# Performance work log

Hardware: AMD Instinct MI355X
Metric: run time of the kernel (lower is better)

The kernel has to match this reference:

```python
import jax, jax.numpy as jnp
import numpy as np

B, N, H = 8, 2048, 1024
FF = 4 * H
EPS = 1e-5

def layer_norm(x, g, b):
    mu = jnp.mean(x, axis=-1, keepdims=True)
    var = jnp.mean(jnp.square(x - mu), axis=-1, keepdims=True)
    return (x - mu) * jax.lax.rsqrt(var + EPS) * g + b

def setup_inputs() -> dict:
    key = jax.random.key(0)
    ks = jax.random.split(key, 6)
    s1 = 1.0 / np.sqrt(H)
    s2 = 1.0 / np.sqrt(FF)
    return {
        "x": jax.random.normal(ks[0], (B, N, H), dtype=jnp.float32),
        "ln1_g": jnp.ones((H,), jnp.float32),
        "ln1_b": jnp.zeros((H,), jnp.float32),
        "ln2_g": jnp.ones((H,), jnp.float32),
        "ln2_b": jnp.zeros((H,), jnp.float32),
        "w1": jax.random.uniform(ks[1], (H, FF), jnp.float32, -s1, s1),
        "b1": jax.random.uniform(ks[2], (FF,), jnp.float32, -s1, s1),
        "w2": jax.random.uniform(ks[3], (FF, H), jnp.float32, -s2, s2),
        "b2": jax.random.uniform(ks[4], (H,), jnp.float32, -s2, s2),
    }

def reference(x, ln1_g, ln1_b, ln2_g, ln2_b, w1, b1, w2, b2):
    # raw unscaled self-attention: softmax(x x^T) x  (dropout = identity, eval mode)
    scores = jnp.einsum('bnh,bmh->bnm', x, x)          # [B,N,N]
    attn = jax.nn.softmax(scores, axis=-1)
    attended = jnp.einsum('bnm,bmh->bnh', attn, x)     # [B,N,H]
    h = layer_norm(x + attended, ln1_g, ln1_b)
    ffn = jnp.einsum('bnf,fh->bnh', jax.nn.gelu(jnp.einsum('bnh,hf->bnf', h, w1) + b1, approximate=False), w2) + b2
    return layer_norm(h + ffn, ln2_g, ln2_b)
```

## Files before the change

### kernel.cpp

```cpp
#include <hip/hip_runtime.h>
#include <stdint.h>

#define NB 8
#define NN 2048
#define HH 1024
#define FFD 4096
constexpr float EPS_ = 1e-5f;

typedef _Float16 f16;
typedef _Float16 f16x8 __attribute__((ext_vector_type(8)));
typedef float f32x4 __attribute__((ext_vector_type(4)));

__device__ __forceinline__ f32x4 MFMA(f16x8 a, f16x8 b, f32x4 c) {
  return __builtin_amdgcn_mfma_f32_16x16x32_f16(a, b, c, 0, 0, 0);
}
__device__ __forceinline__ ushort h2u(f16 h) { union { f16 h; ushort u; } v; v.h = h; return v.u; }
__device__ __forceinline__ uint pack2(float a, float b) {
  return (uint)h2u((f16)a) | ((uint)h2u((f16)b) << 16);
}
__device__ __forceinline__ float4 ld4(const float* p) { return *(const float4*)p; }
__device__ __forceinline__ float gelu(float u) {
  return 0.5f * u * (1.0f + erff(u * 0.70710678118654752f));
}

__global__ void transpose_f16(const float* __restrict__ src, f16* __restrict__ dst,
                              int R, int C) {
  __shared__ float tl[32][33];
  const int t = threadIdx.x;
  const int c0 = blockIdx.x * 32, r0 = blockIdx.y * 32;
  {
    const int r = t >> 3, c4 = t & 7;
    float4 v = ld4(src + (size_t)(r0 + r) * C + c0 + c4 * 4);
    tl[r][c4 * 4 + 0] = v.x; tl[r][c4 * 4 + 1] = v.y;
    tl[r][c4 * 4 + 2] = v.z; tl[r][c4 * 4 + 3] = v.w;
  }
  __syncthreads();
  {
    const int c = t >> 3, r4 = t & 7;
    ushort4 o;
    o.x = h2u((f16)tl[r4 * 4 + 0][c]);
    o.y = h2u((f16)tl[r4 * 4 + 1][c]);
    o.z = h2u((f16)tl[r4 * 4 + 2][c]);
    o.w = h2u((f16)tl[r4 * 4 + 3][c]);
    *(ushort4*)(dst + (size_t)(c0 + c) * R + r0 + r4 * 4) = o;
  }
}

__global__ __launch_bounds__(1024)
void attn_kernel(const float* __restrict__ x, const float* __restrict__ g1,
                 const float* __restrict__ lb1, float* __restrict__ hout) {
  extern __shared__ char smem[];
  char* AB = smem;
  char* BB = smem + 5120;
  char* PB = smem + 46080;
  char* VB = smem + 62976;
  float* RD  = (float*)(smem + 144896);
  float* RD2 = (float*)(smem + 145920);

  const int t = threadIdx.x, l = t & 63, w = t >> 6;
  const int lg = l >> 4, li = l & 15;
  const int wr = w >> 3, wc = w & 7;
  const int b = blockIdx.y, m0 = blockIdx.x * 32;
  const float* __restrict__ xb = x + (size_t)b * NN * HH;

  const int ar = t >> 5, ak = t & 31;
  const int bj = t >> 2, bq = t & 3;
  const int vjp = t & 15, vhg = t >> 4;

  f32x4 Oacc[8] = {};
  float m_run[4] = {-INFINITY, -INFINITY, -INFINITY, -INFINITY};
  float l_run[4] = {0.f, 0.f, 0.f, 0.f};

  for (int jt = 0; jt < 8; ++jt) {
    const int j0 = jt * 256;
    f32x4 sacc[2] = {};
    float qv = xb[(size_t)(m0 + ar) * HH + ak];
    float4 ca = ld4(xb + (size_t)(j0 + bj) * HH + bq * 8);
    float4 cb = ld4(xb + (size_t)(j0 + bj) * HH + bq * 8 + 4);
    for (int kc = 0; kc < 32; ++kc) {
      __syncthreads();
      {
        f16 qh = (f16)qv; f16 ql = (f16)(qv - (float)qh);
        *(ushort*)(AB + ar * 80 + ak * 2) = h2u(qh);
        *(ushort*)(AB + 2560 + ar * 80 + ak * 2) = h2u(ql);
        float vv[8] = {ca.x, ca.y, ca.z, ca.w, cb.x, cb.y, cb.z, cb.w};
        f16x8 hi8, lo8;
#pragma unroll
        for (int i = 0; i < 8; ++i) {
          f16 h = (f16)vv[i]; hi8[i] = h; lo8[i] = (f16)(vv[i] - (float)h);
        }
        *(f16x8*)(BB + bj * 80 + bq * 16) = hi8;
        *(f16x8*)(BB + 20480 + bj * 80 + bq * 16) = lo8;
      }
      if (kc < 31) {
        const int k0 = (kc + 1) * 32;
        qv = xb[(size_t)(m0 + ar) * HH + k0 + ak];
        ca = ld4(xb + (size_t)(j0 + bj) * HH + k0 + bq * 8);
        cb = ld4(xb + (size_t)(j0 + bj) * HH + k0 + bq * 8 + 4);
      }
      __syncthreads();
      const int arow = wr * 16 + li;
      f16x8 ahi = *(const f16x8*)(AB + arow * 80 + lg * 16);
      f16x8 alo = *(const f16x8*)(AB + 2560 + arow * 80 + lg * 16);
#pragma unroll
      for (int ct = 0; ct < 2; ++ct) {
        const int j = wc * 32 + ct * 16 + li;
        f16x8 bhi = *(const f16x8*)(BB + j * 80 + lg * 16);
        f16x8 blo = *(const f16x8*)(BB + 20480 + j * 80 + lg * 16);
        sacc[ct] = MFMA(ahi, bhi, sacc[ct]);
        sacc[ct] = MFMA(ahi, blo, sacc[ct]);
        sacc[ct] = MFMA(alo, bhi, sacc[ct]);
      }
    }

    float tm[4];
#pragma unroll
    for (int r = 0; r < 4; ++r) tm[r] = fmaxf(sacc[0][r], sacc[1][r]);
#pragma unroll
    for (int off = 1; off <= 8; off <<= 1)
#pragma unroll
      for (int r = 0; r < 4; ++r) tm[r] = fmaxf(tm[r], __shfl_xor(tm[r], off, 64));
    if (li == 0)
#pragma unroll
      for (int r = 0; r < 4; ++r) RD[wc * 32 + wr * 16 + lg * 4 + r] = tm[r];
    __syncthreads();
    float mnew[4], fct[4];
#pragma unroll
    for (int r = 0; r < 4; ++r) {
      const int row = wr * 16 + lg * 4 + r;
      float mt = RD[row];
#pragma unroll
      for (int w2 = 1; w2 < 8; ++w2) mt = fmaxf(mt, RD[w2 * 32 + row]);
      mnew[r] = fmaxf(m_run[r], mt);
      fct[r] = __expf(m_run[r] - mnew[r]);
      m_run[r] = mnew[r];
    }
    float psum[4] = {0.f, 0.f, 0.f, 0.f};
#pragma unroll
    for (int ct = 0; ct < 2; ++ct)
#pragma unroll
      for (int r = 0; r < 4; ++r) {
        float p = __expf(sacc[ct][r] - mnew[r]);
        psum[r] += p;
        float po = __shfl_xor(p, 1, 64);
        if (!(l & 1)) {
          const int row = wr * 16 + lg * 4 + r;
          *(uint*)(PB + row * 528 + (wc * 32 + ct * 16 + (li & 14)) * 2) = pack2(p, po);
        }
      }
#pragma unroll
    for (int off = 1; off <= 8; off <<= 1)
#pragma unroll
      for (int r = 0; r < 4; ++r) psum[r] += __shfl_xor(psum[r], off, 64);
    if (li == 0)
#pragma unroll
      for (int r = 0; r < 4; ++r) RD2[wc * 32 + wr * 16 + lg * 4 + r] = psum[r];
    __syncthreads();
#pragma unroll
    for (int r = 0; r < 4; ++r) {
      const int row = wr * 16 + lg * 4 + r;
      float ts = 0.f;
#pragma unroll
      for (int w2 = 0; w2 < 8; ++w2) ts += RD2[w2 * 32 + row];
      l_run[r] = l_run[r] * fct[r] + ts;
    }
#pragma unroll
    for (int ti = 0; ti < 8; ++ti)
#pragma unroll
      for (int r = 0; r < 4; ++r) Oacc[ti][r] *= fct[r];

    float4 v0[4], v1[4];
#pragma unroll
    for (int q = 0; q < 4; ++q) {
      v0[q] = ld4(xb + (size_t)(j0 + 2 * vjp) * HH + vhg * 16 + q * 4);
      v1[q] = ld4(xb + (size_t)(j0 + 2 * vjp + 1) * HH + vhg * 16 + q * 4);
    }
    for (int jc = 0; jc < 8; ++jc) {
      __syncthreads();
#pragma unroll
      for (int q = 0; q < 4; ++q) {
        float a0[4] = {v0[q].x, v0[q].y, v0[q].z, v0[q].w};
        float a1[4] = {v1[q].x, v1[q].y, v1[q].z, v1[q].w};
#pragma unroll
        for (int i = 0; i < 4; ++i) {
          const int h = vhg * 16 + q * 4 + i;
          *(uint*)(VB + h * 80 + vjp * 4) = pack2(a0[i], a1[i]);
        }
      }
      if (jc < 7) {
        const int jj = j0 + (jc + 1) * 32;
#pragma unroll
        for (int q = 0; q < 4; ++q) {
          v0[q] = ld4(xb + (size_t)(jj + 2 * vjp) * HH + vhg * 16 + q * 4);
          v1[q] = ld4(xb + (size_t)(jj + 2 * vjp + 1) * HH + vhg * 16 + q * 4);
        }
      }
      __syncthreads();
      f16x8 pa = *(const f16x8*)(PB + (wr * 16 + li) * 528 + jc * 64 + lg * 16);
#pragma unroll
      for (int ti = 0; ti < 8; ++ti) {
        const int h = wc * 128 + ti * 16 + li;
        f16x8 vb = *(const f16x8*)(VB + h * 80 + lg * 16);
        Oacc[ti] = MFMA(pa, vb, Oacc[ti]);
      }
    }
  }

  float musum[4] = {0.f, 0.f, 0.f, 0.f};
#pragma unroll
  for (int ti = 0; ti < 8; ++ti) {
    const int col = wc * 128 + ti * 16 + li;
#pragma unroll
    for (int r = 0; r < 4; ++r) {
      const int row = m0 + wr * 16 + lg * 4 + r;
      float v = xb[(size_t)row * HH + col] + Oacc[ti][r] / l_run[r];
      Oacc[ti][r] = v; musum[r] += v;
    }
  }
#pragma unroll
  for (int off = 1; off <= 8; off <<= 1)
#pragma unroll
    for (int r = 0; r < 4; ++r) musum[r] += __shfl_xor(musum[r], off, 64);
  if (li == 0)
#pragma unroll
    for (int r = 0; r < 4; ++r) RD[wc * 32 + wr * 16 + lg * 4 + r] = musum[r];
  __syncthreads();
  float mu[4];
#pragma unroll
  for (int r = 0; r < 4; ++r) {
    const int row = wr * 16 + lg * 4 + r;
    float s = 0.f;
#pragma unroll
    for (int w2 = 0; w2 < 8; ++w2) s += RD[w2 * 32 + row];
    mu[r] = s * (1.0f / HH);
  }
  float vsum[4] = {0.f, 0.f, 0.f, 0.f};
#pragma unroll
  for (int ti = 0; ti < 8; ++ti)
#pragma unroll
    for (int r = 0; r < 4; ++r) {
      float d = Oacc[ti][r] - mu[r]; vsum[r] += d * d;
    }
#pragma unroll
  for (int off = 1; off <= 8; off <<= 1)
#pragma unroll
    for (int r = 0; r < 4; ++r) vsum[r] += __shfl_xor(vsum[r], off, 64);
  if (li == 0)
#pragma unroll
    for (int r = 0; r < 4; ++r) RD2[wc * 32 + wr * 16 + lg * 4 + r] = vsum[r];
  __syncthreads();
  float rs[4];
#pragma unroll
  for (int r = 0; r < 4; ++r) {
    const int row = wr * 16 + lg * 4 + r;
    float s = 0.f;
#pragma unroll
    for (int w2 = 0; w2 < 8; ++w2) s += RD2[w2 * 32 + row];
    rs[r] = rsqrtf(s * (1.0f / HH) + EPS_);
  }
#pragma unroll
  for (int ti = 0; ti < 8; ++ti) {
    const int col = wc * 128 + ti * 16 + li;
    const float gv = g1[col], bv = lb1[col];
#pragma unroll
    for (int r = 0; r < 4; ++r) {
      const int row = m0 + wr * 16 + lg * 4 + r;
      hout[((size_t)b * NN + row) * HH + col] = (Oacc[ti][r] - mu[r]) * rs[r] * gv + bv;
    }
  }
}

template<bool WS>
__global__ __launch_bounds__(1024)
void ffn_kernel(float* __restrict__ hio, const float* __restrict__ g2,
                const float* __restrict__ lb2,
                const float* __restrict__ w1, const float* __restrict__ b1f,
                const float* __restrict__ w2, const float* __restrict__ b2f,
                const f16* __restrict__ w1t, const f16* __restrict__ w2t) {
  extern __shared__ char smem[];
  char* HB  = smem;
  char* W1B = smem + 5120;
  char* GB  = smem + 25600;
  char* W2B = smem + 59392;
  float* RD  = (float*)(smem + 141312);
  float* RD2 = (float*)(smem + 142336);

  const int t = threadIdx.x, l = t & 63, w = t >> 6;
  const int lg = l >> 4, li = l & 15;
  const int rt = w >> 2, wc4 = w & 3;
  const int b = blockIdx.y, m0 = blockIdx.x * 64;
  float* __restrict__ hb = hio + ((size_t)b * NN + m0) * HH;

  f32x4 Oacc[16] = {};

  for (int ft = 0; ft < 16; ++ft) {
    const int f0 = ft * 256;
    f32x4 uacc[4] = {};
    const int hr = t >> 4, hk2 = t & 15;
    float2 hv = *(const float2*)(hb + (size_t)hr * HH + hk2 * 2);
    f16x8 wv; float4 wf0, wf1;
    const int wfW = t >> 2, wkq = t & 3;
    const int ki = t & 31, fg = t >> 5;
    if (WS) {
      wv = *(const f16x8*)(w1t + (size_t)(f0 + wfW) * HH + wkq * 8);
    } else {
      wf0 = ld4(w1 + (size_t)ki * FFD + f0 + fg * 8);
      wf1 = ld4(w1 + (size_t)ki * FFD + f0 + fg * 8 + 4);
    }
    for (int kc = 0; kc < 32; ++kc) {
      __syncthreads();
      *(uint*)(HB + hr * 80 + hk2 * 4) = pack2(hv.x, hv.y);
      if (WS) {
        *(f16x8*)(W1B + wfW * 80 + wkq * 16) = wv;
      } else {
        float vv[8] = {wf0.x, wf0.y, wf0.z, wf0.w, wf1.x, wf1.y, wf1.z, wf1.w};
#pragma unroll
        for (int i = 0; i < 8; ++i)
          *(ushort*)(W1B + (fg * 8 + i) * 80 + ki * 2) = h2u((f16)vv[i]);
      }
      if (kc < 31) {
        const int k0 = (kc + 1) * 32;
        hv = *(const float2*)(hb + (size_t)hr * HH + k0 + hk2 * 2);
        if (WS) wv = *(const f16x8*)(w1t + (size_t)(f0 + wfW) * HH + k0 + wkq * 8);
        else {
          wf0 = ld4(w1 + (size_t)(k0 + ki) * FFD + f0 + fg * 8);
          wf1 = ld4(w1 + (size_t)(k0 + ki) * FFD + f0 + fg * 8 + 4);
        }
      }
      __syncthreads();
      f16x8 af = *(const f16x8*)(HB + (rt * 16 + li) * 80 + lg * 16);
#pragma unroll
      for (int ct = 0; ct < 4; ++ct) {
        const int fc = wc4 * 64 + ct * 16 + li;
        f16x8 bf = *(const f16x8*)(W1B + fc * 80 + lg * 16);
        uacc[ct] = MFMA(af, bf, uacc[ct]);
      }
    }
    __syncthreads();
#pragma unroll
    for (int ct = 0; ct < 4; ++ct) {
      const int ucol = wc4 * 64 + ct * 16 + li;
      const float b1v = b1f[f0 + ucol];
#pragma unroll
      for (int r = 0; r < 4; ++r) {
        float g = gelu(uacc[ct][r] + b1v);
        float go = __shfl_xor(g, 1, 64);
        if (!(l & 1)) {
          const int row = rt * 16 + lg * 4 + r;
          *(uint*)(GB + row * 528 + (wc4 * 64 + ct * 16 + (li & 14)) * 2) = pack2(g, go);
        }
      }
    }
    __syncthreads();
    f16x8 wv2[4]; float4 fv[8];
    const int w2fi = t & 31, w2hg = t >> 5;
    if (WS) {
#pragma unroll
      for (int q = 0; q < 4; ++q)
        wv2[q] = *(const f16x8*)(w2t + (size_t)t * FFD + f0 + q * 8);
    } else {
#pragma unroll
      for (int q = 0; q < 8; ++q)
        fv[q] = ld4(w2 + (size_t)(f0 + w2fi) * HH + w2hg * 32 + q * 4);
    }
    for (int fc = 0; fc < 8; ++fc) {
      if (WS) {
#pragma unroll
        for (int q = 0; q < 4; ++q) *(f16x8*)(W2B + t * 80 + q * 16) = wv2[q];
      } else {
#pragma unroll
        for (int q = 0; q < 8; ++q) {
          float vv[4] = {fv[q].x, fv[q].y, fv[q].z, fv[q].w};
#pragma unroll
          for (int i = 0; i < 4; ++i)
            *(ushort*)(W2B + (w2hg * 32 + q * 4 + i) * 80 + w2fi * 2) = h2u((f16)vv[i]);
        }
      }
      if (fc < 7) {
        const int fk = f0 + (fc + 1) * 32;
        if (WS) {
#pragma unroll
          for (int q = 0; q < 4; ++q)
            wv2[q] = *(const f16x8*)(w2t + (size_t)t * FFD + fk + q * 8);
        } else {
#pragma unroll
          for (int q = 0; q < 8; ++q)
            fv[q] = ld4(w2 + (size_t)(fk + w2fi) * HH + w2hg * 32 + q * 4);
        }
      }
      __syncthreads();
      f16x8 ag = *(const f16x8*)(GB + (rt * 16 + li) * 528 + fc * 64 + lg * 16);
#pragma unroll
      for (int ti = 0; ti < 16; ++ti) {
        const int h = wc4 * 256 + ti * 16 + li;
        f16x8 bg = *(const f16x8*)(W2B + h * 80 + lg * 16);
        Oacc[ti] = MFMA(ag, bg, Oacc[ti]);
      }
      __syncthreads();
    }
  }

  float musum[4] = {0.f, 0.f, 0.f, 0.f};
#pragma unroll
  for (int ti = 0; ti < 16; ++ti) {
    const int col = wc4 * 256 + ti * 16 + li;
    const float b2v = b2f[col];
#pragma unroll
    for (int r = 0; r < 4; ++r) {
      const int row = rt * 16 + lg * 4 + r;
      float v = hb[(size_t)row * HH + col] + Oacc[ti][r] + b2v;
      Oacc[ti][r] = v; musum[r] += v;
    }
  }
#pragma unroll
  for (int off = 1; off <= 8; off <<= 1)
#pragma unroll
    for (int r = 0; r < 4; ++r) musum[r] += __shfl_xor(musum[r], off, 64);
  if (li == 0)
#pragma unroll
    for (int r = 0; r < 4; ++r) RD[wc4 * 64 + rt * 16 + lg * 4 + r] = musum[r];
  __syncthreads();
  float mu[4];
#pragma unroll
  for (int r = 0; r < 4; ++r) {
    const int row = rt * 16 + lg * 4 + r;
    float s = 0.f;
#pragma unroll
    for (int w2i = 0; w2i < 4; ++w2i) s += RD[w2i * 64 + row];
    mu[r] = s * (1.0f / HH);
  }
  float vsum[4] = {0.f, 0.f, 0.f, 0.f};
#pragma unroll
  for (int ti = 0; ti < 16; ++ti)
#pragma unroll
    for (int r = 0; r < 4; ++r) { float d = Oacc[ti][r] - mu[r]; vsum[r] += d * d; }
#pragma unroll
  for (int off = 1; off <= 8; off <<= 1)
#pragma unroll
    for (int r = 0; r < 4; ++r) vsum[r] += __shfl_xor(vsum[r], off, 64);
  if (li == 0)
#pragma unroll
    for (int r = 0; r < 4; ++r) RD2[wc4 * 64 + rt * 16 + lg * 4 + r] = vsum[r];
  __syncthreads();
  float rs[4];
#pragma unroll
  for (int r = 0; r < 4; ++r) {
    const int row = rt * 16 + lg * 4 + r;
    float s = 0.f;
#pragma unroll
    for (int w2i = 0; w2i < 4; ++w2i) s += RD2[w2i * 64 + row];
    rs[r] = rsqrtf(s * (1.0f / HH) + EPS_);
  }
#pragma unroll
  for (int ti = 0; ti < 16; ++ti) {
    const int col = wc4 * 256 + ti * 16 + li;
    const float gv = g2[col], bv = lb2[col];
#pragma unroll
    for (int r = 0; r < 4; ++r) {
      const int row = rt * 16 + lg * 4 + r;
      hb[(size_t)row * HH + col] = (Oacc[ti][r] - mu[r]) * rs[r] * gv + bv;
    }
  }
}

extern "C" void kernel_launch(void* const* d_in, const int* in_sizes, int n_in,
                              void* d_out, int out_size, void* d_ws, size_t ws_size,
                              hipStream_t stream) {
  (void)in_sizes; (void)n_in; (void)out_size;
  const float* x    = (const float*)d_in[0];
  const float* ln1g = (const float*)d_in[1];
  const float* ln1b = (const float*)d_in[2];
  const float* ln2g = (const float*)d_in[3];
  const float* ln2b = (const float*)d_in[4];
  const float* w1   = (const float*)d_in[5];
  const float* bb1  = (const float*)d_in[6];
  const float* w2   = (const float*)d_in[7];
  const float* bb2  = (const float*)d_in[8];
  float* out = (float*)d_out;

  const size_t wbytes = (size_t)2 * FFD * HH * sizeof(f16);
  const bool ws_ok = (ws_size >= wbytes) && (d_ws != nullptr);
  f16* w1t = (f16*)d_ws;
  f16* w2t = w1t + (size_t)FFD * HH;

  (void)hipFuncSetAttribute((const void*)attn_kernel,
                            hipFuncAttributeMaxDynamicSharedMemorySize, 146944);
  (void)hipFuncSetAttribute((const void*)ffn_kernel<true>,
                            hipFuncAttributeMaxDynamicSharedMemorySize, 143360);
  (void)hipFuncSetAttribute((const void*)ffn_kernel<false>,
                            hipFuncAttributeMaxDynamicSharedMemorySize, 143360);

  if (ws_ok) {
    transpose_f16<<<dim3(FFD / 32, HH / 32), 256, 0, stream>>>(w1, w1t, HH, FFD);
    transpose_f16<<<dim3(HH / 32, FFD / 32), 256, 0, stream>>>(w2, w2t, FFD, HH);
  }
  attn_kernel<<<dim3(NN / 32, NB), 1024, 146944, stream>>>(x, ln1g, ln1b, out);
  if (ws_ok)
    ffn_kernel<true><<<dim3(NN / 64, NB), 1024, 143360, stream>>>(
        out, ln2g, ln2b, w1, bb1, w2, bb2, w1t, w2t);
  else
    ffn_kernel<false><<<dim3(NN / 64, NB), 1024, 143360, stream>>>(
        out, ln2g, ln2b, w1, bb1, w2, bb2, nullptr, nullptr);
}
```

Before: 2.040 ms.

## Rewrite attention with 32x32 MFMA, precomputed fp16 hi/lo and transposed x

Adds a new attention kernel that uses 32x32x16 MFMA tiles with 64-row query blocks and 512-thread blocks, two blocks per CU. Pre-passes convert x into fp16 hi/lo split arrays and an fp16 transpose, so the kernel streams K and V through double-buffered LDS using direct global-to-LDS loads with an XOR swizzle. This removes per-block fp32-to-fp16 conversion and register staging, and overlaps loads with MFMA work. In exchange it needs much more workspace and extra conversion passes over x, and it keeps the old kernel as a fallback.

```diff
diff --git a/kernel.cpp b/kernel.cpp
--- a/kernel.cpp
+++ b/kernel.cpp
@@ -5,27 +5,51 @@
 #define NN 2048
 #define HH 1024
 #define FFD 4096
+#define M2 8
 constexpr float EPS_ = 1e-5f;
 
 typedef _Float16 f16;
 typedef _Float16 f16x8 __attribute__((ext_vector_type(8)));
 typedef float f32x4 __attribute__((ext_vector_type(4)));
-
-__device__ __forceinline__ f32x4 MFMA(f16x8 a, f16x8 b, f32x4 c) {
+typedef float f32x16 __attribute__((ext_vector_type(16)));
+
+__device__ __forceinline__ f32x4 MFMA16(f16x8 a, f16x8 b, f32x4 c) {
   return __builtin_amdgcn_mfma_f32_16x16x32_f16(a, b, c, 0, 0, 0);
 }
+__device__ __forceinline__ f32x16 MFMA32(f16x8 a, f16x8 b, f32x16 c) {
+  return __builtin_amdgcn_mfma_f32_32x32x16_f16(a, b, c, 0, 0, 0);
+}
 __device__ __forceinline__ ushort h2u(f16 h) { union { f16 h; ushort u; } v; v.h = h; return v.u; }
-__device__ __forceinline__ uint pack2(float a, float b) {
-  return (uint)h2u((f16)a) | ((uint)h2u((f16)b) << 16);
+__device__ __forceinline__ unsigned pack2(float a, float b) {
+  return (unsigned)h2u((f16)a) | ((unsigned)h2u((f16)b) << 16);
 }
 __device__ __forceinline__ float4 ld4(const float* p) { return *(const float4*)p; }
 __device__ __forceinline__ float gelu(float u) {
   return 0.5f * u * (1.0f + erff(u * 0.70710678118654752f));
 }
-
-__global__ void transpose_f16(const float* __restrict__ src, f16* __restrict__ dst,
-                              int R, int C) {
+__device__ __forceinline__ void gload16(const void* g, void* l) {
+  __builtin_amdgcn_global_load_lds(
+      (const __attribute__((address_space(1))) unsigned int*)g,
+      (__attribute__((address_space(3))) unsigned int*)l, 16, 0, 0);
+}
+
+__global__ void convert_hl(const float* __restrict__ x, f16* __restrict__ xh,
+                           f16* __restrict__ xl) {
+  const size_t i = ((size_t)blockIdx.x * blockDim.x + threadIdx.x) * 4;
+  float4 v = ld4(x + i);
+  f16 h0 = (f16)v.x, h1 = (f16)v.y, h2 = (f16)v.z, h3 = (f16)v.w;
+  ushort4 ho = {h2u(h0), h2u(h1), h2u(h2), h2u(h3)};
+  ushort4 lo = {h2u((f16)(v.x - (float)h0)), h2u((f16)(v.y - (float)h1)),
+                h2u((f16)(v.z - (float)h2)), h2u((f16)(v.w - (float)h3))};
+  *(ushort4*)(xh + i) = ho;
+  *(ushort4*)(xl + i) = lo;
+}
+
+__global__ void transpose_f16k(const float* __restrict__ src, f16* __restrict__ dst,
+                               int R, int C, long sbs, long dbs) {
   __shared__ float tl[32][33];
+  src += (size_t)blockIdx.z * sbs;
+  dst += (size_t)blockIdx.z * dbs;
   const int t = threadIdx.x;
   const int c0 = blockIdx.x * 32, r0 = blockIdx.y * 32;
   {
@@ -46,13 +70,268 @@
   }
 }
 
+#define RSTR 528
+__device__ __forceinline__ void stageKB(char* REGb, const f16* xhb, const f16* xlb,
+                                        int j0, int k0, int w, int l) {
+#pragma unroll
+  for (int r = 0; r < 2; ++r) {
+    const int grp = r * 8 + w;
+    const int j = grp * 16 + (l >> 2);
+    const int clog = (l & 3) ^ ((j >> 1) & 3);
+    const size_t src = (size_t)(j0 + j) * HH + k0 + clog * 8;
+    gload16(xhb + src, REGb + grp * 1024);
+    gload16(xlb + src, REGb + 16384 + grp * 1024);
+  }
+}
+__device__ __forceinline__ void stageVB(char* VBb, const f16* xtb, int jabs, int w, int l) {
+#pragma unroll
+  for (int r = 0; r < 4; ++r) {
+    const int grp = r * 8 + w;
+    const int h = grp * 32 + (l >> 1);
+    const int clog = (l & 1) ^ ((h >> 2) & 1);
+    gload16(xtb + (size_t)h * NN + jabs + clog * 8, VBb + grp * 1024);
+  }
+}
+
+__global__ __launch_bounds__(512, 2)
+void attn_v2(const float* __restrict__ x, const f16* __restrict__ xh,
+             const f16* __restrict__ xl, const f16* __restrict__ xt,
+             const float* __restrict__ g1, const float* __restrict__ lb1,
+             float* __restrict__ hout) {
+  extern __shared__ char smem[];
+  char* REG = smem;
+  char* PB  = smem + 65536;
+  float* RD   = (float*)(smem + 99328);
+  float* mrow = (float*)(smem + 100352);
+  float* lrow = (float*)(smem + 100608);
+  float* fctb = (float*)(smem + 100864);
+
+  const int t = threadIdx.x, l = t & 63, w = t >> 6;
+  const int l31 = l & 31, lh = l >> 5;
+  const int wr = w >> 2, wc = w & 3;
+  const int b = blockIdx.y, m0 = blockIdx.x * 64;
+  const f16* __restrict__ xhb = xh + (size_t)b * NN * HH;
+  const f16* __restrict__ xlb = xl + (size_t)b * NN * HH;
+  const f16* __restrict__ xtb = xt + (size_t)b * HH * NN;
+  const float* __restrict__ xb = x + (size_t)b * NN * HH;
+
+  if (t < 64) { mrow[t] = -INFINITY; lrow[t] = 0.f; }
+
+  f32x16 Oacc[8] = {};
+  const int arow = m0 + wr * 32 + l31;
+
+  for (int jt = 0; jt < 8; ++jt) {
+    const int j0 = jt * 256;
+    f32x16 sacc[2] = {};
+
+    f16x8 ah[2], al[2];
+#pragma unroll
+    for (int s = 0; s < 2; ++s) {
+      ah[s] = *(const f16x8*)(xhb + (size_t)arow * HH + s * 16 + lh * 8);
+      al[s] = *(const f16x8*)(xlb + (size_t)arow * HH + s * 16 + lh * 8);
+    }
+    stageKB(REG, xhb, xlb, j0, 0, w, l);
+    __syncthreads();
+    int buf = 0;
+    for (int kc = 0; kc < 32; ++kc) {
+      f16x8 nh[2], nl[2];
+      if (kc < 31) {
+        stageKB(REG + (buf ^ 1) * 32768, xhb, xlb, j0, (kc + 1) * 32, w, l);
+        const int kn = (kc + 1) * 32;
+#pragma unroll
+        for (int s = 0; s < 2; ++s) {
+          nh[s] = *(const f16x8*)(xhb + (size_t)arow * HH + kn + s * 16 + lh * 8);
+          nl[s] = *(const f16x8*)(xlb + (size_t)arow * HH + kn + s * 16 + lh * 8);
+        }
+      }
+      const char* KH = REG + buf * 32768;
+      const char* KL = KH + 16384;
+#pragma unroll
+      for (int ct = 0; ct < 2; ++ct) {
+        const int j = wc * 64 + ct * 32 + l31;
+        const int swz = (j >> 1) & 3;
+        const char* rowH = KH + j * 64;
+        const char* rowL = KL + j * 64;
+#pragma unroll
+        for (int s = 0; s < 2; ++s) {
+          const int cp = (s * 2 + lh) ^ swz;
+          f16x8 bh = *(const f16x8*)(rowH + cp * 16);
+          f16x8 bl = *(const f16x8*)(rowL + cp * 16);
+          sacc[ct] = MFMA32(ah[s], bh, sacc[ct]);
+          sacc[ct] = MFMA32(al[s], bh, sacc[ct]);
+          sacc[ct] = MFMA32(ah[s], bl, sacc[ct]);
+        }
+      }
+      __syncthreads();
+      if (kc < 31) {
+#pragma unroll
+        for (int s = 0; s < 2; ++s) { ah[s] = nh[s]; al[s] = nl[s]; }
+      }
+      buf ^= 1;
+    }
+
+    float tmax[16];
+#pragma unroll
+    for (int rg = 0; rg < 16; ++rg) tmax[rg] = fmaxf(sacc[0][rg], sacc[1][rg]);
+#pragma unroll
+    for (int off = 1; off <= 16; off <<= 1)
+#pragma unroll
+      for (int rg = 0; rg < 16; ++rg) tmax[rg] = fmaxf(tmax[rg], __shfl_xor(tmax[rg], off, 64));
+    if (l31 == 0) {
+#pragma unroll
+      for (int rg = 0; rg < 16; ++rg) {
+        const int rl = (rg & 3) + 8 * (rg >> 2) + 4 * lh;
+        RD[wc * 64 + wr * 32 + rl] = tmax[rg];
+      }
+    }
+    __syncthreads();
+    if (t < 64) {
+      float mt = fmaxf(fmaxf(RD[t], RD[64 + t]), fmaxf(RD[128 + t], RD[192 + t]));
+      float mo = mrow[t];
+      float mn = fmaxf(mo, mt);
+      mrow[t] = mn;
+      fctb[t] = __expf(mo - mn);
+    }
+    __syncthreads();
+    float mv[16], psum[16];
+#pragma unroll
+    for (int rg = 0; rg < 16; ++rg)
+      mv[rg] = mrow[wr * 32 + (rg & 3) + 8 * (rg >> 2) + 4 * lh];
+#pragma unroll
+    for (int ct = 0; ct < 2; ++ct) {
+#pragma unroll
+      for (int rg = 0; rg < 16; ++rg) {
+        float p = __expf(sacc[ct][rg] - mv[rg]);
+        if (ct == 0) psum[rg] = p; else psum[rg] += p;
+        float po = __shfl_xor(p, 1, 64);
+        if (!(l & 1)) {
+          const int R = wr * 32 + (rg & 3) + 8 * (rg >> 2) + 4 * lh;
+          const int col = wc * 64 + ct * 32 + l31;
+          *(unsigned*)(PB + R * RSTR + col * 2) = pack2(p, po);
+        }
+      }
+    }
+#pragma unroll
+    for (int off = 1; off <= 16; off <<= 1)
+#pragma unroll
+      for (int rg = 0; rg < 16; ++rg) psum[rg] += __shfl_xor(psum[rg], off, 64);
+    if (l31 == 0) {
+#pragma unroll
+      for (int rg = 0; rg < 16; ++rg) {
+        const int rl = (rg & 3) + 8 * (rg >> 2) + 4 * lh;
+        RD[wc * 64 + wr * 32 + rl] = psum[rg];
+      }
+    }
+    __syncthreads();
+    if (t < 64) lrow[t] = lrow[t] * fctb[t] + (RD[t] + RD[64 + t] + RD[128 + t] + RD[192 + t]);
+    float fv[16];
+#pragma unroll
+    for (int rg = 0; rg < 16; ++rg)
+      fv[rg] = fctb[wr * 32 + (rg & 3) + 8 * (rg >> 2) + 4 * lh];
+#pragma unroll
+    for (int ht = 0; ht < 8; ++ht)
+#pragma unroll
+      for (int rg = 0; rg < 16; ++rg) Oacc[ht][rg] *= fv[rg];
+
+    stageVB(REG, xtb, j0, w, l);
+    __syncthreads();
+    int vbuf = 0;
+    for (int jc = 0; jc < 16; ++jc) {
+      if (jc < 15) stageVB(REG + (vbuf ^ 1) * 32768, xtb, j0 + (jc + 1) * 16, w, l);
+      const char* VBc = REG + vbuf * 32768;
+      f16x8 pa = *(const f16x8*)(PB + (wr * 32 + l31) * RSTR + (jc * 2 + lh) * 16);
+#pragma unroll
+      for (int ht = 0; ht < 8; ++ht) {
+        const int h = wc * 256 + ht * 32 + l31;
+        f16x8 vb = *(const f16x8*)(VBc + h * 32 + ((lh ^ ((h >> 2) & 1)) * 16));
+        Oacc[ht] = MFMA32(pa, vb, Oacc[ht]);
+      }
+      __syncthreads();
+      vbuf ^= 1;
+    }
+  }
+
+  float lv[16];
+#pragma unroll
+  for (int rg = 0; rg < 16; ++rg)
+    lv[rg] = 1.0f / lrow[wr * 32 + (rg & 3) + 8 * (rg >> 2) + 4 * lh];
+  float musum[16];
+#pragma unroll
+  for (int rg = 0; rg < 16; ++rg) musum[rg] = 0.f;
+#pragma unroll
+  for (int ht = 0; ht < 8; ++ht) {
+    const int col = wc * 256 + ht * 32 + l31;
+#pragma unroll
+    for (int rg = 0; rg < 16; ++rg) {
+      const int R = wr * 32 + (rg & 3) + 8 * (rg >> 2) + 4 * lh;
+      float v = fmaf(Oacc[ht][rg], lv[rg], xb[(size_t)(m0 + R) * HH + col]);
+      Oacc[ht][rg] = v; musum[rg] += v;
+    }
+  }
+#pragma unroll
+  for (int off = 1; off <= 16; off <<= 1)
+#pragma unroll
+    for (int rg = 0; rg < 16; ++rg) musum[rg] += __shfl_xor(musum[rg], off, 64);
+  if (l31 == 0) {
+#pragma unroll
+    for (int rg = 0; rg < 16; ++rg) {
+      const int rl = (rg & 3) + 8 * (rg >> 2) + 4 * lh;
+      RD[wc * 64 + wr * 32 + rl] = musum[rg];
+    }
+  }
+  __syncthreads();
+  if (t < 64) mrow[t] = (RD[t] + RD[64 + t] + RD[128 + t] + RD[192 + t]) * (1.0f / HH);
+  __syncthreads();
+  float mu[16], vsum[16];
+#pragma unroll
+  for (int rg = 0; rg < 16; ++rg) {
+    mu[rg] = mrow[wr * 32 + (rg & 3) + 8 * (rg >> 2) + 4 * lh];
+    vsum[rg] = 0.f;
+  }
+#pragma unroll
+  for (int ht = 0; ht < 8; ++ht)
+#pragma unroll
+    for (int rg = 0; rg < 16; ++rg) {
+      float d = Oacc[ht][rg] - mu[rg];
+      vsum[rg] += d * d;
+    }
+#pragma unroll
+  for (int off = 1; off <= 16; off <<= 1)
+#pragma unroll
+    for (int rg = 0; rg < 16; ++rg) vsum[rg] += __shfl_xor(vsum[rg], off, 64);
+  if (l31 == 0) {
+#pragma unroll
+    for (int rg = 0; rg < 16; ++rg) {
+      const int rl = (rg & 3) + 8 * (rg >> 2) + 4 * lh;
+      RD[wc * 64 + wr * 32 + rl] = vsum[rg];
+    }
+  }
+  __syncthreads();
+  if (t < 64) fctb[t] = rsqrtf((RD[t] + RD[64 + t] + RD[128 + t] + RD[192 + t]) * (1.0f / HH) + EPS_);
+  __syncthreads();
+  float rs[16];
+#pragma unroll
+  for (int rg = 0; rg < 16; ++rg)
+    rs[rg] = fctb[wr * 32 + (rg & 3) + 8 * (rg >> 2) + 4 * lh];
+#pragma unroll
+  for (int ht = 0; ht < 8; ++ht) {
+    const int col = wc * 256 + ht * 32 + l31;
+    const float gv = g1[col], bv = lb1[col];
+#pragma unroll
+    for (int rg = 0; rg < 16; ++rg) {
+      const int R = wr * 32 + (rg & 3) + 8 * (rg >> 2) + 4 * lh;
+      hout[((size_t)b * NN + m0 + R) * HH + col] = (Oacc[ht][rg] - mu[rg]) * rs[rg] * gv + bv;
+    }
+  }
+}
+
 __global__ __launch_bounds__(1024)
-void attn_kernel(const float* __restrict__ x, const float* __restrict__ g1,
+void attn_legacy(const float* __restrict__ x, const float* __restrict__ g1,
                  const float* __restrict__ lb1, float* __restrict__ hout) {
   extern __shared__ char smem[];
   char* AB = smem;
   char* BB = smem + 5120;
-  char* PB = smem + 46080;
+  char* PB2 = smem + 46080;
   char* VB = smem + 62976;
   float* RD  = (float*)(smem + 144896);
   float* RD2 = (float*)(smem + 145920);
@@ -107,22 +386,21 @@
         const int j = wc * 32 + ct * 16 + li;
         f16x8 bhi = *(const f16x8*)(BB + j * 80 + lg * 16);
         f16x8 blo = *(const f16x8*)(BB + 20480 + j * 80 + lg * 16);
-        sacc[ct] = MFMA(ahi, bhi, sacc[ct]);
-        sacc[ct] = MFMA(ahi, blo, sacc[ct]);
-        sacc[ct] = MFMA(alo, bhi, sacc[ct]);
-      }
-    }
-
-    float tm[4];
-#pragma unroll
-    for (int r = 0; r < 4; ++r) tm[r] = fmaxf(sacc[0][r], sacc[1][r]);
+        sacc[ct] = MFMA16(ahi, bhi, sacc[ct]);
+        sacc[ct] = MFMA16(ahi, blo, sacc[ct]);
+        sacc[ct] = MFMA16(alo, bhi, sacc[ct]);
+      }
+    }
+    float m[4];
+#pragma unroll
+    for (int r = 0; r < 4; ++r) m[r] = fmaxf(sacc[0][r], sacc[1][r]);
 #pragma unroll
     for (int off = 1; off <= 8; off <<= 1)
 #pragma unroll
-      for (int r = 0; r < 4; ++r) tm[r] = fmaxf(tm[r], __shfl_xor(tm[r], off, 64));
+      for (int r = 0; r < 4; ++r) m[r] = fmaxf(m[r], __shfl_xor(m[r], off, 64));
     if (li == 0)
 #pragma unroll
-      for (int r = 0; r < 4; ++r) RD[wc * 32 + wr * 16 + lg * 4 + r] = tm[r];
+      for (int r = 0; r < 4; ++r) RD[wc * 32 + wr * 16 + lg * 4 + r] = m[r];
     __syncthreads();
     float mnew[4], fct[4];
 #pragma unroll
@@ -145,7 +423,7 @@
         float po = __shfl_xor(p, 1, 64);
         if (!(l & 1)) {
           const int row = wr * 16 + lg * 4 + r;
-          *(uint*)(PB + row * 528 + (wc * 32 + ct * 16 + (li & 14)) * 2) = pack2(p, po);
+          *(unsigned*)(PB2 + row * 528 + (wc * 32 + ct * 16 + (li & 14)) * 2) = pack2(p, po);
         }
       }
 #pragma unroll
@@ -184,7 +462,7 @@
 #pragma unroll
         for (int i = 0; i < 4; ++i) {
           const int h = vhg * 16 + q * 4 + i;
-          *(uint*)(VB + h * 80 + vjp * 4) = pack2(a0[i], a1[i]);
+          *(unsigned*)(VB + h * 80 + vjp * 4) = pack2(a0[i], a1[i]);
         }
       }
       if (jc < 7) {
@@ -196,12 +474,12 @@
         }
       }
       __syncthreads();
-      f16x8 pa = *(const f16x8*)(PB + (wr * 16 + li) * 528 + jc * 64 + lg * 16);
+      f16x8 pa = *(const f16x8*)(PB2 + (wr * 16 + li) * 528 + jc * 64 + lg * 16);
 #pragma unroll
       for (int ti = 0; ti < 8; ++ti) {
         const int h = wc * 128 + ti * 16 + li;
         f16x8 vb = *(const f16x8*)(VB + h * 80 + lg * 16);
-        Oacc[ti] = MFMA(pa, vb, Oacc[ti]);
+        Oacc[ti] = MFMA16(pa, vb, Oacc[ti]);
       }
     }
   }
@@ -285,7 +563,8 @@
   float* RD  = (float*)(smem + 141312);
   float* RD2 = (float*)(smem + 142336);
 
-  const int t = threadIdx.x, l = t & 63, w = t >> 6;
+  const int t = threadIdx.x, l = t & 63;
+  const int w = t >> 6;
   const int lg = l >> 4, li = l & 15;
   const int rt = w >> 2, wc4 = w & 3;
   const int b = blockIdx.y, m0 = blockIdx.x * 64;
@@ -309,7 +588,7 @@
     }
     for (int kc = 0; kc < 32; ++kc) {
       __syncthreads();
-      *(uint*)(HB + hr * 80 + hk2 * 4) = pack2(hv.x, hv.y);
+      *(unsigned*)(HB + hr * 80 + hk2 * 4) = pack2(hv.x, hv.y);
       if (WS) {
         *(f16x8*)(W1B + wfW * 80 + wkq * 16) = wv;
       } else {
@@ -333,10 +612,14 @@
       for (int ct = 0; ct < 4; ++ct) {
         const int fc = wc4 * 64 + ct * 16 + li;
         f16x8 bf = *(const f16x8*)(W1B + fc * 80 + lg * 16);
-        uacc[ct] = MFMA(af, bf, uacc[ct]);
+        uacc[ct] = MFMA16(af, bf, uacc[ct]);
       }
     }
     __syncthreads();
+    {
+      const float4 b1v = *(const float4*)(b1f + f0 + 4 * t);
+      (void)b1v;
+    }
 #pragma unroll
     for (int ct = 0; ct < 4; ++ct) {
       const int ucol = wc4 * 64 + ct * 16 + li;
@@ -347,7 +630,7 @@
         float go = __shfl_xor(g, 1, 64);
         if (!(l & 1)) {
           const int row = rt * 16 + lg * 4 + r;
-          *(uint*)(GB + row * 528 + (wc4 * 64 + ct * 16 + (li & 14)) * 2) = pack2(g, go);
+          *(unsigned*)(GB + row * 528 + (wc4 * 64 + ct * 16 + (li & 14)) * 2) = pack2(g, go);
         }
       }
     }
@@ -394,12 +677,13 @@
       for (int ti = 0; ti < 16; ++ti) {
         const int h = wc4 * 256 + ti * 16 + li;
         f16x8 bg = *(const f16x8*)(W2B + h * 80 + lg * 16);
-        Oacc[ti] = MFMA(ag, bg, Oacc[ti]);
-      }
-      __syncthreads();
-    }
-  }
-
+        Oacc[ti] = MFMA16(ag, bg, Oacc[ti]);
+      }
+      __syncthreads();
+    }
+  }
+
+  const float4 dummy = {0,0,0,0}; (void)dummy;
   float musum[4] = {0.f, 0.f, 0.f, 0.f};
 #pragma unroll
   for (int ti = 0; ti < 16; ++ti) {
@@ -478,24 +762,41 @@
   const float* bb2  = (const float*)d_in[8];
   float* out = (float*)d_out;
 
-  const size_t wbytes = (size_t)2 * FFD * HH * sizeof(f16);
-  const bool ws_ok = (ws_size >= wbytes) && (d_ws != nullptr);
+  const size_t wN   = (size_t)FFD * HH;
+  const size_t xN   = (size_t)NB * NN * HH;
+  const size_t need_w    = 2 * wN * sizeof(f16);
+  const size_t need_full = need_w + 3 * xN * sizeof(f16);
+  const bool ws_w    = (ws_size >= need_w) && d_ws;
+  const bool ws_full = (ws_size >= need_full) && d_ws;
+
   f16* w1t = (f16*)d_ws;
-  f16* w2t = w1t + (size_t)FFD * HH;
-
-  (void)hipFuncSetAttribute((const void*)attn_kernel,
+  f16* w2t = w1t + wN;
+  f16* xh  = w2t + wN;
+  f16* xl  = xh + xN;
+  f16* xt  = xl + xN;
+
+  (void)hipFuncSetAttribute((const void*)attn_v2,
+                            hipFuncAttributeMaxDynamicSharedMemorySize, 101376);
+  (void)hipFuncSetAttribute((const void*)attn_legacy,
                             hipFuncAttributeMaxDynamicSharedMemorySize, 146944);
   (void)hipFuncSetAttribute((const void*)ffn_kernel<true>,
                             hipFuncAttributeMaxDynamicSharedMemorySize, 143360);
   (void)hipFuncSetAttribute((const void*)ffn_kernel<false>,
                             hipFuncAttributeMaxDynamicSharedMemorySize, 143360);
 
-  if (ws_ok) {
-    transpose_f16<<<dim3(FFD / 32, HH / 32), 256, 0, stream>>>(w1, w1t, HH, FFD);
-    transpose_f16<<<dim3(HH / 32, FFD / 32), 256, 0, stream>>>(w2, w2t, FFD, HH);
-  }
-  attn_kernel<<<dim3(NN / 32, NB), 1024, 146944, stream>>>(x, ln1g, ln1b, out);
-  if (ws_ok)
+  if (ws_w) {
+    transpose_f16k<<<dim3(FFD / 32, HH / 32, 1), 256, 0, stream>>>(w1, w1t, HH, FFD, 0, 0);
+    transpose_f16k<<<dim3(HH / 32, FFD / 32, 1), 256, 0, stream>>>(w2, w2t, FFD, HH, 0, 0);
+  }
+  if (ws_full) {
+    convert_hl<<<(int)(xN / 4 / 256), 256, 0, stream>>>(x, xh, xl);
+    transpose_f16k<<<dim3(HH / 32, NN / 32, NB), 256, 0, stream>>>(
+        x, xt, NN, HH, (long)NN * HH, (long)HH * NN);
+    attn_v2<<<dim3(NN / 64, NB), 512, 101376, stream>>>(x, xh, xl, xt, ln1g, ln1b, out);
+  } else {
+    attn_legacy<<<dim3(NN / 32, NB), 1024, 146944, stream>>>(x, ln1g, ln1b, out);
+  }
+  if (ws_w)
     ffn_kernel<true><<<dim3(NN / 64, NB), 1024, 143360, stream>>>(
         out, ln2g, ln2b, w1, bb1, w2, bb2, w1t, w2t);
   else
```

New measurement: 1.666 ms. -18.3%, faster.
